# Kernel optimization log

Hardware: AMD Instinct MI355X
Metric: run time of the kernel (lower is better)

Reference implementation:

```python
import jax, jax.numpy as jnp
import numpy as np

N, D_IN, D_OUT = 4096, 1024, 1024

def setup_inputs() -> dict:
    key = jax.random.key(0)
    ks = jax.random.split(key, 7)
    s = 1.0 / np.sqrt(D_IN)
    return {
        "x": jax.random.normal(ks[0], (N, D_IN), dtype=jnp.float32),
        "W1": jax.random.normal(ks[1], (D_OUT, D_IN), dtype=jnp.float32) * s,
        "b1": jax.random.normal(ks[2], (D_OUT,), dtype=jnp.float32) * 0.01,
        "W2": jax.random.normal(ks[3], (D_OUT, D_IN), dtype=jnp.float32) * s,
        "b2": jax.random.normal(ks[4], (D_OUT,), dtype=jnp.float32) * 0.01,
        "W3": jax.random.normal(ks[5], (D_OUT, D_IN), dtype=jnp.float32) * s,
        "b3": jax.random.normal(ks[6], (D_OUT,), dtype=jnp.float32) * 0.01,
        "output_dim": D_OUT,
    }

def reference(x, W1, b1, W2, b2, W3, b3, output_dim):
    # q, k, v: [N, D_OUT]  (torch Linear: x @ W.T + b)
    q = x @ W1.T + b1
    k = x @ W2.T + b2
    v = x @ W3.T + b3
    # NOTE: original computes K @ Q^T (not Q @ K^T) — keep faithful.
    scale = 1.0 / jnp.sqrt(jnp.asarray(output_dim, dtype=x.dtype))
    attn = jax.nn.softmax(jnp.einsum("nd,md->nm", k, q) * scale, axis=-1)  # [N, N]
    # value.unsqueeze(0) * attn.unsqueeze(-1) summed over axis 1 == attn @ v
    return attn @ v  # [N, D_OUT]
```

## Files before the change

### kernel.cpp

```cpp
#include <hip/hip_runtime.h>


typedef short bf16x8 __attribute__((ext_vector_type(8)));
typedef float f32x4  __attribute__((ext_vector_type(4)));

__device__ __forceinline__ short f2bf(float f) {
    unsigned u = __builtin_bit_cast(unsigned, f);
    u += 0x7FFFu + ((u >> 16) & 1u);
    return (short)(u >> 16);
}
__device__ __forceinline__ float bf2f(short s) {
    return __builtin_bit_cast(float, (unsigned)((unsigned short)s) << 16);
}

__device__ __forceinline__ void gld_lds16(const short* g, short* l) {
    __builtin_amdgcn_global_load_lds(
        (const __attribute__((address_space(1))) void*)g,
        (__attribute__((address_space(3))) void*)l, 16, 0, 0);
}

template<int BM, int BN>
__global__ __launch_bounds__(256)
void gemm_bt(const short* __restrict__ A, int lda,
             const short* __restrict__ B, int ldb,
             const float* __restrict__ bias, int bias_mode,
             void* __restrict__ Cout, int ldc, int c_fp32, float scale,
             int K, size_t zstride)
{
    constexpr int NT = BN / 32;
    __shared__ __align__(16) short As[BM * 64];
    __shared__ __align__(16) short Bs[BN * 64];

    const int tid  = threadIdx.x;
    const int lane = tid & 63;
    const int wave = tid >> 6;
    const int wm   = (wave >> 1) * 64;
    const int wn   = (wave & 1) * (BN / 2);
    const int quad = lane >> 4;
    const int l16  = lane & 15;
    const size_t bm0 = (size_t)blockIdx.y * BM;
    const size_t bn0 = (size_t)blockIdx.x * BN;
    const int koff = blockIdx.z * K;

    f32x4 acc[4][NT] = {};

    const int srow = lane >> 3;
    const int scol = ((lane & 7) ^ srow) << 3;
    const short* Ag = A + (bm0 + srow) * (size_t)lda + koff + scol;
    const short* Bg = B + (bn0 + srow) * (size_t)ldb + koff + scol;

    for (int k0 = 0; k0 < K; k0 += 64) {
#pragma unroll
        for (int cc = 0; cc < BM / 8; cc += 4) {
            const int c = cc + wave;
            gld_lds16(Ag + (size_t)c * 8 * lda + k0, &As[c * 512]);
        }
#pragma unroll
        for (int cc = 0; cc < BN / 8; cc += 4) {
            const int c = cc + wave;
            gld_lds16(Bg + (size_t)c * 8 * ldb + k0, &Bs[c * 512]);
        }
        __syncthreads();

        bf16x8 af[2][4], bfr[2][NT];
#pragma unroll
        for (int ks = 0; ks < 2; ks++) {
            const int sw = (ks << 2) + quad;
#pragma unroll
            for (int mt = 0; mt < 4; mt++) {
                const int r = wm + mt * 16 + l16;
                af[ks][mt] = *(const bf16x8*)(&As[r * 64 + ((sw ^ (r & 7)) << 3)]);
            }
#pragma unroll
            for (int nt = 0; nt < NT; nt++) {
                const int r = wn + nt * 16 + l16;
                bfr[ks][nt] = *(const bf16x8*)(&Bs[r * 64 + ((sw ^ (r & 7)) << 3)]);
            }
        }
#pragma unroll
        for (int ks = 0; ks < 2; ks++)
#pragma unroll
            for (int mt = 0; mt < 4; mt++)
#pragma unroll
                for (int nt = 0; nt < NT; nt++)
                    acc[mt][nt] = __builtin_amdgcn_mfma_f32_16x16x32_bf16(
                        af[ks][mt], bfr[ks][nt], acc[mt][nt], 0, 0, 0);
        __syncthreads();
    }

    float* Cf = (float*)Cout + blockIdx.z * zstride;
    short* Cs = (short*)Cout + blockIdx.z * zstride;
#pragma unroll
    for (int mt = 0; mt < 4; mt++) {
#pragma unroll
        for (int nt = 0; nt < NT; nt++) {
            const size_t col = bn0 + wn + nt * 16 + l16;
            const float bcol = (bias_mode == 1) ? bias[col] : 0.0f;
#pragma unroll
            for (int r = 0; r < 4; r++) {
                const size_t row = bm0 + wm + mt * 16 + quad * 4 + r;
                float v = acc[mt][nt][r] * scale + bcol;
                if (bias_mode == 2) v += bias[row];
                if (c_fp32) Cf[row * (size_t)ldc + col] = v;
                else        Cs[row * (size_t)ldc + col] = f2bf(v);
            }
        }
    }
}

__global__ __launch_bounds__(256)
void softmax_rows_bf16(short* __restrict__ P)
{
    short* p = P + (size_t)blockIdx.x * 4096;
    const int tid = threadIdx.x;
    const int wave = tid >> 6, lane = tid & 63;
    const int base = tid << 4;

    short sh[16];
    *(int4*)(sh)     = *(const int4*)(p + base);
    *(int4*)(sh + 8) = *(const int4*)(p + base + 8);

    float v[16];
    float mx = -1e30f;
#pragma unroll
    for (int i = 0; i < 16; i++) { v[i] = bf2f(sh[i]); mx = fmaxf(mx, v[i]); }
#pragma unroll
    for (int off = 32; off; off >>= 1) mx = fmaxf(mx, __shfl_down(mx, off));
    __shared__ float red[4];
    if (lane == 0) red[wave] = mx;
    __syncthreads();
    mx = fmaxf(fmaxf(red[0], red[1]), fmaxf(red[2], red[3]));

    float sum = 0.0f;
#pragma unroll
    for (int i = 0; i < 16; i++) { v[i] = __expf(v[i] - mx); sum += v[i]; }
#pragma unroll
    for (int off = 32; off; off >>= 1) sum += __shfl_down(sum, off);
    __syncthreads();
    if (lane == 0) red[wave] = sum;
    __syncthreads();
    const float inv = 1.0f / (red[0] + red[1] + red[2] + red[3]);

#pragma unroll
    for (int i = 0; i < 16; i++) sh[i] = f2bf(v[i] * inv);
    *(int4*)(p + base)     = *(const int4*)(sh);
    *(int4*)(p + base + 8) = *(const int4*)(sh + 8);
}

__global__ __launch_bounds__(256)
void transpose_v(const short* __restrict__ qkv, short* __restrict__ vt)
{
    __shared__ short sh[64][72];
    const int n0 = blockIdx.x * 64, d0 = blockIdx.y * 64;
    const int t = threadIdx.x;
    const int r = t >> 2, c = (t & 3) << 4;

    const short* src = qkv + (size_t)(n0 + r) * 3072 + 2048 + d0 + c;
    *(int4*)(&sh[r][c])     = *(const int4*)(src);
    *(int4*)(&sh[r][c + 8]) = *(const int4*)(src + 8);
    __syncthreads();

    short tmp[16];
#pragma unroll
    for (int j = 0; j < 16; j++) tmp[j] = sh[c + j][r];
    short* dst = vt + (size_t)(d0 + r) * 4096 + n0 + c;
    *(int4*)(dst)     = *(const int4*)(tmp);
    *(int4*)(dst + 8) = *(const int4*)(tmp + 8);
}

__global__ __launch_bounds__(256)
void reduce2(const float* __restrict__ p, float* __restrict__ out, int n4)
{
    const int i = blockIdx.x * 256 + threadIdx.x;
    if (i >= n4) return;
    const float4 a = ((const float4*)p)[i];
    const float4 b = ((const float4*)(p + (size_t)4096 * 1024))[i];
    float4 o;
    o.x = a.x + b.x; o.y = a.y + b.y; o.z = a.z + b.z; o.w = a.w + b.w;
    ((float4*)out)[i] = o;
}

__global__ __launch_bounds__(256)
void cast4(const float* __restrict__ in, short* __restrict__ out, int n4)
{
    const int i = blockIdx.x * 256 + threadIdx.x;
    if (i >= n4) return;
    const float4 f = ((const float4*)in)[i];
    short4 o;
    o.x = f2bf(f.x); o.y = f2bf(f.y); o.z = f2bf(f.z); o.w = f2bf(f.w);
    ((short4*)out)[i] = o;
}

__global__ __launch_bounds__(256)
void cast_w3(const float* __restrict__ W1, const float* __restrict__ W2,
             const float* __restrict__ W3, short* __restrict__ out, int per4)
{
    const int i = blockIdx.x * 256 + threadIdx.x;
    if (i >= 3 * per4) return;
    const float* src = (i < per4) ? W1 : (i < 2 * per4 ? W2 : W3);
    const int j = (i < per4) ? i : (i < 2 * per4 ? i - per4 : i - 2 * per4);
    const float4 f = ((const float4*)src)[j];
    short4 o;
    o.x = f2bf(f.x); o.y = f2bf(f.y); o.z = f2bf(f.z); o.w = f2bf(f.w);
    ((short4*)out)[i] = o;
}

__global__ __launch_bounds__(256)
void bias_cat3(const float* __restrict__ b1, const float* __restrict__ b2,
               const float* __restrict__ b3, float* __restrict__ cat, int n)
{
    const int i = blockIdx.x * 256 + threadIdx.x;
    if (i < n) cat[i] = b1[i];
    else if (i < 2 * n) cat[i] = b2[i - n];
    else if (i < 3 * n) cat[i] = b3[i - 2 * n];
}

extern "C" void kernel_launch(void* const* d_in, const int* in_sizes, int n_in,
                              void* d_out, int out_size, void* d_ws, size_t ws_size,
                              hipStream_t stream)
{
    const float* x  = (const float*)d_in[0];
    const float* W1 = (const float*)d_in[1];
    const float* b1 = (const float*)d_in[2];
    const float* W2 = (const float*)d_in[3];
    const float* b2 = (const float*)d_in[4];
    const float* W3 = (const float*)d_in[5];
    const float* b3 = (const float*)d_in[6];
    float* out = (float*)d_out;

    const int N = 4096, D = 1024;

    short* xb   = (short*)d_ws;
    short* Wb   = xb + (size_t)N * D;
    float* bcat = (float*)(Wb + (size_t)3 * D * D);
    short* qkv  = (short*)(bcat + 3 * D);
    short* vt   = qkv + (size_t)N * 3 * D;
    short* S    = vt + (size_t)N * D;
    float* outp = (float*)d_ws;

    cast4<<<(N * D / 4) / 256, 256, 0, stream>>>(x, xb, N * D / 4);
    cast_w3<<<(3 * D * D / 4) / 256, 256, 0, stream>>>(W1, W2, W3, Wb, D * D / 4);
    bias_cat3<<<(3 * D + 255) / 256, 256, 0, stream>>>(b1, b2, b3, bcat, D);

    dim3 gqkv(3 * D / 128, N / 128);
    gemm_bt<128, 128><<<gqkv, 256, 0, stream>>>(xb, D, Wb, D, bcat, 1,
                                                qkv, 3 * D, 0, 1.0f, D, 0);

    dim3 gt(N / 64, D / 64);
    transpose_v<<<gt, 256, 0, stream>>>(qkv, vt);

    dim3 gs(N / 128, N / 128);
    gemm_bt<128, 128><<<gs, 256, 0, stream>>>(qkv + D, 3 * D, qkv, 3 * D,
                                              nullptr, 0, S, N, 0, 0.03125f,
                                              D, 0);

    softmax_rows_bf16<<<N, 256, 0, stream>>>(S);

    dim3 go(D / 64, N / 128, 2);
    gemm_bt<128, 64><<<go, 256, 0, stream>>>(S, N, vt, N, nullptr, 0,
                                             outp, D, 1, 1.0f, N / 2,
                                             (size_t)N * D);

    reduce2<<<(N * D / 4) / 256, 256, 0, stream>>>(outp, out, N * D / 4);
}
```

Before: 259.5 us.

## Fuse exp into score GEMM, defer softmax normalization, merge prep kernels

```diff
diff --git a/kernel.cpp b/kernel.cpp
--- a/kernel.cpp
+++ b/kernel.cpp
@@ -23,8 +23,8 @@
 __global__ __launch_bounds__(256)
 void gemm_bt(const short* __restrict__ A, int lda,
              const short* __restrict__ B, int ldb,
-             const float* __restrict__ bias, int bias_mode,
-             void* __restrict__ Cout, int ldc, int c_fp32, float scale,
+             const float* __restrict__ bias,
+             short* __restrict__ Cout, int ldc, int cmode, float scale,
              int K, size_t zstride)
 {
     constexpr int NT = BN / 32;
@@ -62,89 +62,46 @@
         }
         __syncthreads();
 
-        bf16x8 af[2][4], bfr[2][NT];
 #pragma unroll
         for (int ks = 0; ks < 2; ks++) {
             const int sw = (ks << 2) + quad;
+            bf16x8 af[4], bfr[NT];
 #pragma unroll
             for (int mt = 0; mt < 4; mt++) {
                 const int r = wm + mt * 16 + l16;
-                af[ks][mt] = *(const bf16x8*)(&As[r * 64 + ((sw ^ (r & 7)) << 3)]);
+                af[mt] = *(const bf16x8*)(&As[r * 64 + ((sw ^ (r & 7)) << 3)]);
             }
 #pragma unroll
             for (int nt = 0; nt < NT; nt++) {
                 const int r = wn + nt * 16 + l16;
-                bfr[ks][nt] = *(const bf16x8*)(&Bs[r * 64 + ((sw ^ (r & 7)) << 3)]);
+                bfr[nt] = *(const bf16x8*)(&Bs[r * 64 + ((sw ^ (r & 7)) << 3)]);
             }
-        }
-#pragma unroll
-        for (int ks = 0; ks < 2; ks++)
 #pragma unroll
             for (int mt = 0; mt < 4; mt++)
 #pragma unroll
                 for (int nt = 0; nt < NT; nt++)
                     acc[mt][nt] = __builtin_amdgcn_mfma_f32_16x16x32_bf16(
-                        af[ks][mt], bfr[ks][nt], acc[mt][nt], 0, 0, 0);
+                        af[mt], bfr[nt], acc[mt][nt], 0, 0, 0);
+        }
         __syncthreads();
     }
 
-    float* Cf = (float*)Cout + blockIdx.z * zstride;
-    short* Cs = (short*)Cout + blockIdx.z * zstride;
+    short* Cs = Cout + ((cmode == 3) ? blockIdx.z * zstride : 0);
 #pragma unroll
     for (int mt = 0; mt < 4; mt++) {
 #pragma unroll
         for (int nt = 0; nt < NT; nt++) {
             const size_t col = bn0 + wn + nt * 16 + l16;
-            const float bcol = (bias_mode == 1) ? bias[col] : 0.0f;
+            const float bc = bias ? bias[col] : 0.0f;
 #pragma unroll
             for (int r = 0; r < 4; r++) {
                 const size_t row = bm0 + wm + mt * 16 + quad * 4 + r;
-                float v = acc[mt][nt][r] * scale + bcol;
-                if (bias_mode == 2) v += bias[row];
-                if (c_fp32) Cf[row * (size_t)ldc + col] = v;
-                else        Cs[row * (size_t)ldc + col] = f2bf(v);
+                float v = acc[mt][nt][r] * scale + bc;
+                if (cmode == 2) v = __expf(v);
+                Cs[row * (size_t)ldc + col] = f2bf(v);
             }
         }
     }
-}
-
-__global__ __launch_bounds__(256)
-void softmax_rows_bf16(short* __restrict__ P)
-{
-    short* p = P + (size_t)blockIdx.x * 4096;
-    const int tid = threadIdx.x;
-    const int wave = tid >> 6, lane = tid & 63;
-    const int base = tid << 4;
-
-    short sh[16];
-    *(int4*)(sh)     = *(const int4*)(p + base);
-    *(int4*)(sh + 8) = *(const int4*)(p + base + 8);
-
-    float v[16];
-    float mx = -1e30f;
-#pragma unroll
-    for (int i = 0; i < 16; i++) { v[i] = bf2f(sh[i]); mx = fmaxf(mx, v[i]); }
-#pragma unroll
-    for (int off = 32; off; off >>= 1) mx = fmaxf(mx, __shfl_down(mx, off));
-    __shared__ float red[4];
-    if (lane == 0) red[wave] = mx;
-    __syncthreads();
-    mx = fmaxf(fmaxf(red[0], red[1]), fmaxf(red[2], red[3]));
-
-    float sum = 0.0f;
-#pragma unroll
-    for (int i = 0; i < 16; i++) { v[i] = __expf(v[i] - mx); sum += v[i]; }
-#pragma unroll
-    for (int off = 32; off; off >>= 1) sum += __shfl_down(sum, off);
-    __syncthreads();
-    if (lane == 0) red[wave] = sum;
-    __syncthreads();
-    const float inv = 1.0f / (red[0] + red[1] + red[2] + red[3]);
-
-#pragma unroll
-    for (int i = 0; i < 16; i++) sh[i] = f2bf(v[i] * inv);
-    *(int4*)(p + base)     = *(const int4*)(sh);
-    *(int4*)(p + base + 8) = *(const int4*)(sh + 8);
 }
 
 __global__ __launch_bounds__(256)
@@ -169,50 +126,66 @@
 }
 
 __global__ __launch_bounds__(256)
-void reduce2(const float* __restrict__ p, float* __restrict__ out, int n4)
+void reduce4div(const short* __restrict__ E, const short* __restrict__ outp,
+                float* __restrict__ out)
+{
+    const int row = blockIdx.x;
+    const int t = threadIdx.x;
+    const int wave = t >> 6, lane = t & 63;
+
+    const short* e = E + (size_t)row * 4096 + (t << 4);
+    short sh[16];
+    *(int4*)(sh)     = *(const int4*)(e);
+    *(int4*)(sh + 8) = *(const int4*)(e + 8);
+    float s = 0.0f;
+#pragma unroll
+    for (int i = 0; i < 16; i++) s += bf2f(sh[i]);
+#pragma unroll
+    for (int off = 32; off; off >>= 1) s += __shfl_down(s, off);
+    __shared__ float red[4];
+    if (lane == 0) red[wave] = s;
+    __syncthreads();
+    const float inv = 1.0f / (red[0] + red[1] + red[2] + red[3]);
+
+    const size_t base = (size_t)row * 1024 + (t << 2);
+    float a[4] = {0.0f, 0.0f, 0.0f, 0.0f};
+#pragma unroll
+    for (int z = 0; z < 4; z++) {
+        short4 p = *(const short4*)(outp + z * (size_t)4096 * 1024 + base);
+        a[0] += bf2f(p.x); a[1] += bf2f(p.y);
+        a[2] += bf2f(p.z); a[3] += bf2f(p.w);
+    }
+    float4 o;
+    o.x = a[0] * inv; o.y = a[1] * inv; o.z = a[2] * inv; o.w = a[3] * inv;
+    *(float4*)(out + base) = o;
+}
+
+__global__ __launch_bounds__(256)
+void prep(const float* __restrict__ x, const float* __restrict__ W1,
+          const float* __restrict__ W2, const float* __restrict__ W3,
+          const float* __restrict__ b1, const float* __restrict__ b2,
+          const float* __restrict__ b3,
+          short* __restrict__ xb, short* __restrict__ Wb,
+          float* __restrict__ bcat)
 {
     const int i = blockIdx.x * 256 + threadIdx.x;
-    if (i >= n4) return;
-    const float4 a = ((const float4*)p)[i];
-    const float4 b = ((const float4*)(p + (size_t)4096 * 1024))[i];
-    float4 o;
-    o.x = a.x + b.x; o.y = a.y + b.y; o.z = a.z + b.z; o.w = a.w + b.w;
-    ((float4*)out)[i] = o;
-}
-
-__global__ __launch_bounds__(256)
-void cast4(const float* __restrict__ in, short* __restrict__ out, int n4)
-{
-    const int i = blockIdx.x * 256 + threadIdx.x;
-    if (i >= n4) return;
-    const float4 f = ((const float4*)in)[i];
-    short4 o;
-    o.x = f2bf(f.x); o.y = f2bf(f.y); o.z = f2bf(f.z); o.w = f2bf(f.w);
-    ((short4*)out)[i] = o;
-}
-
-__global__ __launch_bounds__(256)
-void cast_w3(const float* __restrict__ W1, const float* __restrict__ W2,
-             const float* __restrict__ W3, short* __restrict__ out, int per4)
-{
-    const int i = blockIdx.x * 256 + threadIdx.x;
-    if (i >= 3 * per4) return;
-    const float* src = (i < per4) ? W1 : (i < 2 * per4 ? W2 : W3);
-    const int j = (i < per4) ? i : (i < 2 * per4 ? i - per4 : i - 2 * per4);
-    const float4 f = ((const float4*)src)[j];
-    short4 o;
-    o.x = f2bf(f.x); o.y = f2bf(f.y); o.z = f2bf(f.z); o.w = f2bf(f.w);
-    ((short4*)out)[i] = o;
-}
-
-__global__ __launch_bounds__(256)
-void bias_cat3(const float* __restrict__ b1, const float* __restrict__ b2,
-               const float* __restrict__ b3, float* __restrict__ cat, int n)
-{
-    const int i = blockIdx.x * 256 + threadIdx.x;
-    if (i < n) cat[i] = b1[i];
-    else if (i < 2 * n) cat[i] = b2[i - n];
-    else if (i < 3 * n) cat[i] = b3[i - 2 * n];
+    const int NX = 1048576;
+    const int NW = 262144;
+    if (i < NX + 3 * NW) {
+        const float* src; short* dst; int j;
+        if (i < NX)               { src = x;  dst = xb; j = i; }
+        else if (i < NX + NW)     { src = W1; dst = Wb; j = i - NX; }
+        else if (i < NX + 2 * NW) { src = W2; dst = Wb + 1048576; j = i - NX - NW; }
+        else                      { src = W3; dst = Wb + 2097152; j = i - NX - 2 * NW; }
+        const float4 f = ((const float4*)src)[j];
+        short4 o;
+        o.x = f2bf(f.x); o.y = f2bf(f.y); o.z = f2bf(f.z); o.w = f2bf(f.w);
+        *(short4*)(dst + (j << 2)) = o;
+    } else {
+        const int j = i - (NX + 3 * NW);
+        if (j < 3072)
+            bcat[j] = (j < 1024) ? b1[j] : (j < 2048 ? b2[j - 1024] : b3[j - 2048]);
+    }
 }
 
 extern "C" void kernel_launch(void* const* d_in, const int* in_sizes, int n_in,
@@ -230,36 +203,33 @@
 
     const int N = 4096, D = 1024;
 
-    short* xb   = (short*)d_ws;
-    short* Wb   = xb + (size_t)N * D;
-    float* bcat = (float*)(Wb + (size_t)3 * D * D);
-    short* qkv  = (short*)(bcat + 3 * D);
-    short* vt   = qkv + (size_t)N * 3 * D;
-    short* S    = vt + (size_t)N * D;
-    float* outp = (float*)d_ws;
-
-    cast4<<<(N * D / 4) / 256, 256, 0, stream>>>(x, xb, N * D / 4);
-    cast_w3<<<(3 * D * D / 4) / 256, 256, 0, stream>>>(W1, W2, W3, Wb, D * D / 4);
-    bias_cat3<<<(3 * D + 255) / 256, 256, 0, stream>>>(b1, b2, b3, bcat, D);
-
-    dim3 gqkv(3 * D / 128, N / 128);
-    gemm_bt<128, 128><<<gqkv, 256, 0, stream>>>(xb, D, Wb, D, bcat, 1,
-                                                qkv, 3 * D, 0, 1.0f, D, 0);
+    char* wsb = (char*)d_ws;
+    short* vt   = (short*)wsb;
+    short* E    = (short*)(wsb + (size_t)8  * 1024 * 1024);
+    short* xb   = (short*)(wsb + (size_t)40 * 1024 * 1024);
+    short* Wb   = (short*)(wsb + (size_t)48 * 1024 * 1024);
+    float* bcat = (float*)(wsb + (size_t)54 * 1024 * 1024);
+    short* qkv  = (short*)(wsb + (size_t)54 * 1024 * 1024 + 16384);
+    short* outp = (short*)(wsb + (size_t)40 * 1024 * 1024);
+
+    prep<<<(1048576 + 3 * 262144 + 3072 + 255) / 256, 256, 0, stream>>>(
+        x, W1, W2, W3, b1, b2, b3, xb, Wb, bcat);
+
+    dim3 gqkv(3 * D / 96, N / 128);
+    gemm_bt<128, 96><<<gqkv, 256, 0, stream>>>(xb, D, Wb, D, bcat,
+                                               qkv, 3 * D, 0, 1.0f, D, 0);
 
     dim3 gt(N / 64, D / 64);
     transpose_v<<<gt, 256, 0, stream>>>(qkv, vt);
 
     dim3 gs(N / 128, N / 128);
     gemm_bt<128, 128><<<gs, 256, 0, stream>>>(qkv + D, 3 * D, qkv, 3 * D,
-                                              nullptr, 0, S, N, 0, 0.03125f,
-                                              D, 0);
-
-    softmax_rows_bf16<<<N, 256, 0, stream>>>(S);
-
-    dim3 go(D / 64, N / 128, 2);
-    gemm_bt<128, 64><<<go, 256, 0, stream>>>(S, N, vt, N, nullptr, 0,
-                                             outp, D, 1, 1.0f, N / 2,
-                                             (size_t)N * D);
-
-    reduce2<<<(N * D / 4) / 256, 256, 0, stream>>>(outp, out, N * D / 4);
-}
+                                              nullptr, E, N, 2, 0.03125f, D, 0);
+
+    dim3 go(D / 128, N / 128, 4);
+    gemm_bt<128, 128><<<go, 256, 0, stream>>>(E, N, vt, N, nullptr,
+                                              outp, D, 3, 1.0f, N / 4,
+                                              (size_t)N * D);
+
+    reduce4div<<<N, 256, 0, stream>>>(E, outp, out);
+}
```

Measured after the change: 245.4 us. -5.4%, faster.
